# Optimization experiments

Hardware: AMD Instinct MI355X
Metric: run time of the kernel (lower is better)

The kernel has to match this reference:

```python
import jax, jax.numpy as jnp
import numpy as np

EMBED = 1024
HEADS = 16
HEAD_DIM = EMBED // HEADS


def setup_inputs() -> dict:
    key = jax.random.key(0)
    ks = jax.random.split(key, 8)
    B, S = 2, 2048
    inp = {
        "values": jax.random.normal(ks[0], (B, S, EMBED), jnp.float32),
        "keys": jax.random.normal(ks[1], (B, S, EMBED), jnp.float32),
        "queries": jax.random.normal(ks[2], (B, S, EMBED), jnp.float32),
        # per-head projection weights (torch Linear: y = x @ W.T), shared across heads
        "Wv": jax.random.normal(ks[3], (HEAD_DIM, HEAD_DIM), jnp.float32) / np.sqrt(HEAD_DIM),
        "Wk": jax.random.normal(ks[4], (HEAD_DIM, HEAD_DIM), jnp.float32) / np.sqrt(HEAD_DIM),
        "Wq": jax.random.normal(ks[5], (HEAD_DIM, HEAD_DIM), jnp.float32) / np.sqrt(HEAD_DIM),
        "Wo": jax.random.normal(ks[6], (EMBED, EMBED), jnp.float32) / np.sqrt(EMBED),
        "bo": jax.random.normal(ks[7], (EMBED,), jnp.float32) * 0.02,
    }
    return inp


def reference(values, keys, queries, Wv, Wk, Wq, Wo, bo):
    B, S, _ = queries.shape
    # split heads: (B, H, S, D)
    def split(x):
        return x.reshape(B, -1, HEADS, HEAD_DIM).transpose(0, 2, 1, 3)
    v, k, q = split(values), split(keys), split(queries)
    # per-head linear projections (no bias): x @ W.T
    v = jnp.einsum('bhsd,ed->bhse', v, Wv)
    k = jnp.einsum('bhsd,ed->bhse', k, Wk)
    q = jnp.einsum('bhsd,ed->bhse', q, Wq)
    # scaled dot-product attention (naive, full matrix)
    scores = jnp.einsum('bhqd,bhkd->bhqk', q, k) / jnp.sqrt(jnp.float32(HEAD_DIM))
    attn = jax.nn.softmax(scores, axis=-1)
    out = jnp.einsum('bhqk,bhkd->bhqd', attn, v)
    # merge heads and output projection
    out = out.transpose(0, 2, 1, 3).reshape(B, S, EMBED)
    return out @ Wo.T + bo
```

## Files before the change

### kernel.cpp

```cpp
#include <hip/hip_runtime.h>
#include <stdint.h>

#define HEADS 16
#define HD    64
#define SEQ   2048
#define BATCH 2
#define EMB   1024

using short8  = __attribute__((ext_vector_type(8))) short;
using float4v = __attribute__((ext_vector_type(4))) float;

__device__ __forceinline__ unsigned int f2bfr(float f) {
    return (__float_as_uint(f) + 0x8000u) >> 16;
}

__device__ __forceinline__ unsigned int dpp_xor1(unsigned int x) {
    return (unsigned int)__builtin_amdgcn_update_dpp(0, (int)x, 0xB1, 0xF, 0xF, true);
}

__global__ __launch_bounds__(256) void cvt_wo_kernel(const float* __restrict__ Wo,
                                                     unsigned short* __restrict__ Wob) {
    int i = (blockIdx.x * 256 + threadIdx.x) * 4;
    float4 v = *(const float4*)(Wo + i);
    uint2 o;
    o.x = f2bfr(v.x) | (f2bfr(v.y) << 16);
    o.y = f2bfr(v.z) | (f2bfr(v.w) << 16);
    *(uint2*)(Wob + i) = o;
}

__global__ __launch_bounds__(256) void proj_kernel(
    const float* __restrict__ Vx, const float* __restrict__ Kx, const float* __restrict__ Qx,
    const float* __restrict__ Wv, const float* __restrict__ Wk, const float* __restrict__ Wq,
    unsigned short* __restrict__ Qp, unsigned short* __restrict__ Kp,
    unsigned short* __restrict__ Vt) {
    __shared__ __align__(16) unsigned short Ws[64 * 72];
    __shared__ __align__(16) unsigned short xs[64 * 72];
    __shared__ __align__(16) unsigned short vt2[64 * 72];

    const int t = threadIdx.x, w = t >> 6, lane = t & 63, cl = lane & 15, quad = lane >> 4;
    const int z  = blockIdx.z;
    const int bh = blockIdx.y;
    const int b  = bh >> 4, h = bh & 15;
    const int s0 = blockIdx.x * 64;

    const float* x = (z == 0) ? Qx : (z == 1) ? Kx : Vx;
    const float* W = (z == 0) ? Wq : (z == 1) ? Wk : Wv;
    const float scale = (z == 0) ? 0.18033688011112044f : 1.0f;

#pragma unroll
    for (int rep = 0; rep < 4; ++rep) {
        int idx = rep * 1024 + t * 4;
        int e = idx >> 6, d0 = idx & 63;
        float4 w4 = *(const float4*)(W + idx);
        uint2 pk;
        pk.x = f2bfr(w4.x * scale) | (f2bfr(w4.y * scale) << 16);
        pk.y = f2bfr(w4.z * scale) | (f2bfr(w4.w * scale) << 16);
        *(uint2*)(&Ws[e * 72 + d0]) = pk;

        int s = e;
        float4 v4 = *(const float4*)(x + (size_t)(b * SEQ + s0 + s) * EMB + h * 64 + d0);
        uint2 px;
        px.x = f2bfr(v4.x) | (f2bfr(v4.y) << 16);
        px.y = f2bfr(v4.z) | (f2bfr(v4.w) << 16);
        *(uint2*)(&xs[s * 72 + d0]) = px;
    }
    __syncthreads();

    short8 a0 = *(const short8*)(&xs[(w * 16 + cl) * 72 + quad * 8]);
    short8 a1 = *(const short8*)(&xs[(w * 16 + cl) * 72 + 32 + quad * 8]);
    float4v c[4];
#pragma unroll
    for (int nt = 0; nt < 4; ++nt) c[nt] = (float4v){0.f, 0.f, 0.f, 0.f};
#pragma unroll
    for (int nt = 0; nt < 4; ++nt) {
        short8 b0 = *(const short8*)(&Ws[(nt * 16 + cl) * 72 + quad * 8]);
        c[nt] = __builtin_amdgcn_mfma_f32_16x16x32_bf16(a0, b0, c[nt], 0, 0, 0);
        short8 b1 = *(const short8*)(&Ws[(nt * 16 + cl) * 72 + 32 + quad * 8]);
        c[nt] = __builtin_amdgcn_mfma_f32_16x16x32_bf16(a1, b1, c[nt], 0, 0, 0);
    }

    if (z < 2) {
#pragma unroll
        for (int nt = 0; nt < 4; ++nt)
#pragma unroll
            for (int r = 0; r < 4; ++r)
                xs[(w * 16 + quad * 4 + r) * 72 + nt * 16 + cl] =
                    (unsigned short)f2bfr(c[nt][r]);
        unsigned short* outp = (z == 0) ? Qp : Kp;
        int sl = w * 16 + (lane >> 2), c0 = (lane & 3) * 16;
        uint4 o0 = *(const uint4*)(&xs[sl * 72 + c0]);
        uint4 o1 = *(const uint4*)(&xs[sl * 72 + c0 + 8]);
        size_t base = ((size_t)bh * SEQ + s0 + sl) * 64 + c0;
        *(uint4*)(outp + base)     = o0;
        *(uint4*)(outp + base + 8) = o1;
    } else {
#pragma unroll
        for (int nt = 0; nt < 4; ++nt)
#pragma unroll
            for (int r = 0; r < 4; ++r)
                vt2[(nt * 16 + cl) * 72 + w * 16 + quad * 4 + r] =
                    (unsigned short)f2bfr(c[nt][r]);
        __syncthreads();
        int e = t >> 2, sc0 = (t & 3) * 16;
        uint4 o0 = *(const uint4*)(&vt2[e * 72 + sc0]);
        uint4 o1 = *(const uint4*)(&vt2[e * 72 + sc0 + 8]);
        size_t base = ((size_t)bh * 64 + e) * SEQ + s0 + sc0;
        *(uint4*)(Vt + base)     = o0;
        *(uint4*)(Vt + base + 8) = o1;
    }
}

__global__ __launch_bounds__(256) void attn_kernel(
    const unsigned short* __restrict__ Qp, const unsigned short* __restrict__ Kp,
    const unsigned short* __restrict__ Vt, unsigned short* __restrict__ AO) {
    __shared__ __align__(16) unsigned short Ks[2][64 * 72];
    __shared__ __align__(16) unsigned short Vs[2][64 * 72];
    __shared__ __align__(16) unsigned short Ps[4][32 * 72];

    const int t = threadIdx.x;
    const int w = t >> 6, lane = t & 63, cl = lane & 15, quad = lane >> 4;
    const int bh = blockIdx.y;
    const int q0 = blockIdx.x * 128;
    const size_t hbase = (size_t)bh * SEQ * 64;
    const unsigned short* Kbase = Kp + hbase;
    const unsigned short* Vbase = Vt + hbase;

    short8 aq[2][2];
#pragma unroll
    for (int qt = 0; qt < 2; ++qt) {
        size_t rbase = hbase + (size_t)(q0 + w * 32 + qt * 16 + cl) * 64 + quad * 8;
        aq[qt][0] = *(const short8*)(Qp + rbase);
        aq[qt][1] = *(const short8*)(Qp + rbase + 32);
    }

    short8 ones;
#pragma unroll
    for (int i = 0; i < 8; ++i) ones[i] = (short)0x3F80;

    float4v acc[2][5];
#pragma unroll
    for (int qt = 0; qt < 2; ++qt)
#pragma unroll
        for (int nt = 0; nt < 5; ++nt) acc[qt][nt] = (float4v){0.f, 0.f, 0.f, 0.f};

    const int srow = t >> 3;
    const int scol = (t & 7) * 8;

    uint4 kreg[2], vreg[2];
#pragma unroll
    for (int p = 0; p < 2; ++p) {
        int row = srow + p * 32;
        kreg[p] = *(const uint4*)(Kbase + row * 64 + scol);
        vreg[p] = *(const uint4*)(Vbase + (size_t)row * SEQ + scol);
    }

    const int even = ((lane & 1) == 0);
    const unsigned int psel = even ? 0x03020706u : 0x07060302u;
    const int evoff = even ? 0 : 16;
    unsigned int* Pw = (unsigned int*)Ps[w];

    for (int kc = 0; kc < SEQ / 64; ++kc) {
        const int buf = kc & 1;
#pragma unroll
        for (int p = 0; p < 2; ++p) {
            int row = srow + p * 32;
            *(uint4*)(&Ks[buf][row * 72 + scol]) = kreg[p];
            *(uint4*)(&Vs[buf][row * 72 + scol]) = vreg[p];
        }
        __syncthreads();
        if (kc + 1 < SEQ / 64) {
#pragma unroll
            for (int p = 0; p < 2; ++p) {
                int row = srow + p * 32;
                kreg[p] = *(const uint4*)(Kbase + (size_t)(kc + 1) * 4096 + row * 64 + scol);
                vreg[p] = *(const uint4*)(Vbase + (size_t)row * SEQ + (kc + 1) * 64 + scol);
            }
        }

        float4v c[2][4];
#pragma unroll
        for (int qt = 0; qt < 2; ++qt)
#pragma unroll
            for (int nt = 0; nt < 4; ++nt) c[qt][nt] = (float4v){0.f, 0.f, 0.f, 0.f};
#pragma unroll
        for (int nt = 0; nt < 4; ++nt) {
            short8 bk0 = *(const short8*)(&Ks[buf][(nt * 16 + cl) * 72 + quad * 8]);
            short8 bk1 = *(const short8*)(&Ks[buf][(nt * 16 + cl) * 72 + 32 + quad * 8]);
            c[0][nt] = __builtin_amdgcn_mfma_f32_16x16x32_bf16(aq[0][0], bk0, c[0][nt], 0, 0, 0);
            c[0][nt] = __builtin_amdgcn_mfma_f32_16x16x32_bf16(aq[0][1], bk1, c[0][nt], 0, 0, 0);
            c[1][nt] = __builtin_amdgcn_mfma_f32_16x16x32_bf16(aq[1][0], bk0, c[1][nt], 0, 0, 0);
            c[1][nt] = __builtin_amdgcn_mfma_f32_16x16x32_bf16(aq[1][1], bk1, c[1][nt], 0, 0, 0);
        }

#pragma unroll
        for (int qt = 0; qt < 2; ++qt) {
#pragma unroll
            for (int r = 0; r < 4; ++r) {
                unsigned int rr[4], wd[4];
#pragma unroll
                for (int nt = 0; nt < 4; ++nt)
                    rr[nt] = __float_as_uint(__builtin_amdgcn_exp2f(c[qt][nt][r])) + 0x8000u;
#pragma unroll
                for (int nt = 0; nt < 4; ++nt) {
                    unsigned int nb = dpp_xor1(rr[nt]);
                    wd[nt] = __builtin_amdgcn_perm(rr[nt], nb, psel);
                }
                unsigned int wa = even ? wd[0] : wd[2];
                unsigned int wb = even ? wd[1] : wd[3];
                int dwbase = (qt * 16 + quad * 4 + r) * 36 + evoff + (cl >> 1);
                Pw[dwbase]     = wa;
                Pw[dwbase + 8] = wb;
            }
        }

#pragma unroll
        for (int s2i = 0; s2i < 2; ++s2i) {
            short8 ap0 = *(const short8*)(&Ps[w][cl * 72 + s2i * 32 + quad * 8]);
            short8 ap1 = *(const short8*)(&Ps[w][(16 + cl) * 72 + s2i * 32 + quad * 8]);
#pragma unroll
            for (int nt = 0; nt < 4; ++nt) {
                short8 bv = *(const short8*)(&Vs[buf][(nt * 16 + cl) * 72 + s2i * 32 + quad * 8]);
                acc[0][nt] = __builtin_amdgcn_mfma_f32_16x16x32_bf16(ap0, bv, acc[0][nt], 0, 0, 0);
                acc[1][nt] = __builtin_amdgcn_mfma_f32_16x16x32_bf16(ap1, bv, acc[1][nt], 0, 0, 0);
            }
            acc[0][4] = __builtin_amdgcn_mfma_f32_16x16x32_bf16(ap0, ones, acc[0][4], 0, 0, 0);
            acc[1][4] = __builtin_amdgcn_mfma_f32_16x16x32_bf16(ap1, ones, acc[1][4], 0, 0, 0);
        }
    }

#pragma unroll
    for (int qt = 0; qt < 2; ++qt) {
        float inv[4];
#pragma unroll
        for (int r = 0; r < 4; ++r) inv[r] = 1.0f / acc[qt][4][r];
#pragma unroll
        for (int nt = 0; nt < 4; ++nt) {
#pragma unroll
            for (int r = 0; r < 4; ++r) {
                int row = q0 + w * 32 + qt * 16 + quad * 4 + r;
                AO[hbase + (size_t)row * 64 + nt * 16 + cl] =
                    (unsigned short)f2bfr(acc[qt][nt][r] * inv[r]);
            }
        }
    }
}

__global__ __launch_bounds__(256) void outproj_kernel(
    const unsigned short* __restrict__ AO, const unsigned short* __restrict__ Wob,
    const float* __restrict__ bo, float* __restrict__ out) {
    __shared__ __align__(16) unsigned short As[2][64 * 72];
    __shared__ __align__(16) unsigned short Bs[2][64 * 72];

    const int t = threadIdx.x, w = t >> 6, lane = t & 63, cl = lane & 15, quad = lane >> 4;
    const int e0 = blockIdx.x * 64;
    const int m0 = blockIdx.y * 64;
    const int srow = t >> 3, scol = (t & 7) * 8;

    float4v c[4];
#pragma unroll
    for (int nt = 0; nt < 4; ++nt) c[nt] = (float4v){0.f, 0.f, 0.f, 0.f};

    uint4 areg[2], breg[2];
#pragma unroll
    for (int p = 0; p < 2; ++p) {
        int i = srow + p * 32;
        int r = m0 + i, b = r >> 11, s = r & 2047;
        areg[p] = *(const uint4*)(AO + ((size_t)(b * 16 + 0) * SEQ + s) * 64 + scol);
        breg[p] = *(const uint4*)(Wob + (size_t)(e0 + i) * EMB + scol);
    }

    for (int hc = 0; hc < 16; ++hc) {
        const int buf = hc & 1;
#pragma unroll
        for (int p = 0; p < 2; ++p) {
            int i = srow + p * 32;
            *(uint4*)(&As[buf][i * 72 + scol]) = areg[p];
            *(uint4*)(&Bs[buf][i * 72 + scol]) = breg[p];
        }
        __syncthreads();
        if (hc + 1 < 16) {
#pragma unroll
            for (int p = 0; p < 2; ++p) {
                int i = srow + p * 32;
                int r = m0 + i, b = r >> 11, s = r & 2047;
                areg[p] = *(const uint4*)(AO + ((size_t)(b * 16 + hc + 1) * SEQ + s) * 64 + scol);
                breg[p] = *(const uint4*)(Wob + (size_t)(e0 + i) * EMB + (hc + 1) * 64 + scol);
            }
        }
#pragma unroll
        for (int s2i = 0; s2i < 2; ++s2i) {
            short8 a = *(const short8*)(&As[buf][(w * 16 + cl) * 72 + s2i * 32 + quad * 8]);
#pragma unroll
            for (int nt = 0; nt < 4; ++nt) {
                short8 bb = *(const short8*)(&Bs[buf][(nt * 16 + cl) * 72 + s2i * 32 + quad * 8]);
                c[nt] = __builtin_amdgcn_mfma_f32_16x16x32_bf16(a, bb, c[nt], 0, 0, 0);
            }
        }
    }

#pragma unroll
    for (int nt = 0; nt < 4; ++nt) {
        float bias = bo[e0 + nt * 16 + cl];
#pragma unroll
        for (int r = 0; r < 4; ++r) {
            int row = m0 + w * 16 + quad * 4 + r;
            out[(size_t)row * EMB + e0 + nt * 16 + cl] = c[nt][r] + bias;
        }
    }
}

extern "C" void kernel_launch(void* const* d_in, const int* in_sizes, int n_in,
                              void* d_out, int out_size, void* d_ws, size_t ws_size,
                              hipStream_t stream) {
    const float* values  = (const float*)d_in[0];
    const float* keys    = (const float*)d_in[1];
    const float* queries = (const float*)d_in[2];
    const float* Wv = (const float*)d_in[3];
    const float* Wk = (const float*)d_in[4];
    const float* Wq = (const float*)d_in[5];
    const float* Wo = (const float*)d_in[6];
    const float* bo = (const float*)d_in[7];
    float* out = (float*)d_out;

    char* ws = (char*)d_ws;
    unsigned short* Qp  = (unsigned short*)(ws);
    unsigned short* Kp  = (unsigned short*)(ws + (8u  << 20));
    unsigned short* Vt  = (unsigned short*)(ws + (16u << 20));
    unsigned short* AO  = (unsigned short*)(ws + (24u << 20));
    unsigned short* Wob = (unsigned short*)(ws + (32u << 20));

    cvt_wo_kernel<<<dim3(1024), dim3(256), 0, stream>>>(Wo, Wob);
    proj_kernel<<<dim3(SEQ / 64, BATCH * HEADS, 3), dim3(256), 0, stream>>>(
        values, keys, queries, Wv, Wk, Wq, Qp, Kp, Vt);
    attn_kernel<<<dim3(SEQ / 128, BATCH * HEADS), dim3(256), 0, stream>>>(Qp, Kp, Vt, AO);
    outproj_kernel<<<dim3(EMB / 64, (BATCH * SEQ) / 64), dim3(256), 0, stream>>>(
        AO, Wob, bo, out);
}
```

Before: 262.6 us.

## Load K/V fragments directly from global in attention, fuse Wo conversion into projection

The attention kernel no longer stages K and V tiles through shared memory with double buffering and block barriers. Each wave now loads its MFMA B-operand fragments straight from global memory, relying on L1/L2 reuse across the four waves. The P write layout is changed to match, the grid is transposed so blocks sharing a head run together, and launch bounds request two blocks per CU. The separate Wo-to-bf16 conversion kernel is folded into the projection launch as an extra z slice, saving one launch. The risk is redundant global/L2 traffic, since every wave now reloads the same K/V data.

```diff
diff --git a/kernel.cpp b/kernel.cpp
--- a/kernel.cpp
+++ b/kernel.cpp
@@ -18,21 +18,12 @@
     return (unsigned int)__builtin_amdgcn_update_dpp(0, (int)x, 0xB1, 0xF, 0xF, true);
 }
 
-__global__ __launch_bounds__(256) void cvt_wo_kernel(const float* __restrict__ Wo,
-                                                     unsigned short* __restrict__ Wob) {
-    int i = (blockIdx.x * 256 + threadIdx.x) * 4;
-    float4 v = *(const float4*)(Wo + i);
-    uint2 o;
-    o.x = f2bfr(v.x) | (f2bfr(v.y) << 16);
-    o.y = f2bfr(v.z) | (f2bfr(v.w) << 16);
-    *(uint2*)(Wob + i) = o;
-}
-
 __global__ __launch_bounds__(256) void proj_kernel(
     const float* __restrict__ Vx, const float* __restrict__ Kx, const float* __restrict__ Qx,
     const float* __restrict__ Wv, const float* __restrict__ Wk, const float* __restrict__ Wq,
+    const float* __restrict__ Wo,
     unsigned short* __restrict__ Qp, unsigned short* __restrict__ Kp,
-    unsigned short* __restrict__ Vt) {
+    unsigned short* __restrict__ Vt, unsigned short* __restrict__ Wob) {
     __shared__ __align__(16) unsigned short Ws[64 * 72];
     __shared__ __align__(16) unsigned short xs[64 * 72];
     __shared__ __align__(16) unsigned short vt2[64 * 72];
@@ -42,6 +33,16 @@
     const int bh = blockIdx.y;
     const int b  = bh >> 4, h = bh & 15;
     const int s0 = blockIdx.x * 64;
+
+    if (z == 3) {
+        int idx = (bh * 32 + blockIdx.x) * 1024 + t * 4;
+        float4 v = *(const float4*)(Wo + idx);
+        uint2 o;
+        o.x = f2bfr(v.x) | (f2bfr(v.y) << 16);
+        o.y = f2bfr(v.z) | (f2bfr(v.w) << 16);
+        *(uint2*)(Wob + idx) = o;
+        return;
+    }
 
     const float* x = (z == 0) ? Qx : (z == 1) ? Kx : Vx;
     const float* W = (z == 0) ? Wq : (z == 1) ? Wk : Wv;
@@ -110,17 +111,15 @@
     }
 }
 
-__global__ __launch_bounds__(256) void attn_kernel(
+__global__ __launch_bounds__(256, 2) void attn_kernel(
     const unsigned short* __restrict__ Qp, const unsigned short* __restrict__ Kp,
     const unsigned short* __restrict__ Vt, unsigned short* __restrict__ AO) {
-    __shared__ __align__(16) unsigned short Ks[2][64 * 72];
-    __shared__ __align__(16) unsigned short Vs[2][64 * 72];
     __shared__ __align__(16) unsigned short Ps[4][32 * 72];
 
     const int t = threadIdx.x;
     const int w = t >> 6, lane = t & 63, cl = lane & 15, quad = lane >> 4;
-    const int bh = blockIdx.y;
-    const int q0 = blockIdx.x * 128;
+    const int bh = blockIdx.x;
+    const int q0 = blockIdx.y * 128;
     const size_t hbase = (size_t)bh * SEQ * 64;
     const unsigned short* Kbase = Kp + hbase;
     const unsigned short* Vbase = Vt + hbase;
@@ -143,37 +142,23 @@
 #pragma unroll
         for (int nt = 0; nt < 5; ++nt) acc[qt][nt] = (float4v){0.f, 0.f, 0.f, 0.f};
 
-    const int srow = t >> 3;
-    const int scol = (t & 7) * 8;
-
-    uint4 kreg[2], vreg[2];
-#pragma unroll
-    for (int p = 0; p < 2; ++p) {
-        int row = srow + p * 32;
-        kreg[p] = *(const uint4*)(Kbase + row * 64 + scol);
-        vreg[p] = *(const uint4*)(Vbase + (size_t)row * SEQ + scol);
-    }
-
     const int even = ((lane & 1) == 0);
     const unsigned int psel = even ? 0x03020706u : 0x07060302u;
-    const int evoff = even ? 0 : 16;
+    const int evoff = even ? 0 : 8;
     unsigned int* Pw = (unsigned int*)Ps[w];
 
+    const unsigned short* kptr = Kbase + (size_t)(cl * 64 + quad * 8);
+    const unsigned short* vptr = Vbase + (size_t)cl * SEQ + quad * 8;
+
+#pragma unroll 2
     for (int kc = 0; kc < SEQ / 64; ++kc) {
-        const int buf = kc & 1;
-#pragma unroll
-        for (int p = 0; p < 2; ++p) {
-            int row = srow + p * 32;
-            *(uint4*)(&Ks[buf][row * 72 + scol]) = kreg[p];
-            *(uint4*)(&Vs[buf][row * 72 + scol]) = vreg[p];
-        }
-        __syncthreads();
-        if (kc + 1 < SEQ / 64) {
-#pragma unroll
-            for (int p = 0; p < 2; ++p) {
-                int row = srow + p * 32;
-                kreg[p] = *(const uint4*)(Kbase + (size_t)(kc + 1) * 4096 + row * 64 + scol);
-                vreg[p] = *(const uint4*)(Vbase + (size_t)row * SEQ + (kc + 1) * 64 + scol);
+        short8 kf[4][2], vf[4][2];
+#pragma unroll
+        for (int nt = 0; nt < 4; ++nt) {
+#pragma unroll
+            for (int s2 = 0; s2 < 2; ++s2) {
+                kf[nt][s2] = *(const short8*)(kptr + (size_t)(kc * 64 + nt * 16) * 64 + s2 * 32);
+                vf[nt][s2] = *(const short8*)(vptr + (size_t)(nt * 16) * SEQ + kc * 64 + s2 * 32);
             }
         }
 
@@ -184,12 +169,10 @@
             for (int nt = 0; nt < 4; ++nt) c[qt][nt] = (float4v){0.f, 0.f, 0.f, 0.f};
 #pragma unroll
         for (int nt = 0; nt < 4; ++nt) {
-            short8 bk0 = *(const short8*)(&Ks[buf][(nt * 16 + cl) * 72 + quad * 8]);
-            short8 bk1 = *(const short8*)(&Ks[buf][(nt * 16 + cl) * 72 + 32 + quad * 8]);
-            c[0][nt] = __builtin_amdgcn_mfma_f32_16x16x32_bf16(aq[0][0], bk0, c[0][nt], 0, 0, 0);
-            c[0][nt] = __builtin_amdgcn_mfma_f32_16x16x32_bf16(aq[0][1], bk1, c[0][nt], 0, 0, 0);
-            c[1][nt] = __builtin_amdgcn_mfma_f32_16x16x32_bf16(aq[1][0], bk0, c[1][nt], 0, 0, 0);
-            c[1][nt] = __builtin_amdgcn_mfma_f32_16x16x32_bf16(aq[1][1], bk1, c[1][nt], 0, 0, 0);
+            c[0][nt] = __builtin_amdgcn_mfma_f32_16x16x32_bf16(aq[0][0], kf[nt][0], c[0][nt], 0, 0, 0);
+            c[0][nt] = __builtin_amdgcn_mfma_f32_16x16x32_bf16(aq[0][1], kf[nt][1], c[0][nt], 0, 0, 0);
+            c[1][nt] = __builtin_amdgcn_mfma_f32_16x16x32_bf16(aq[1][0], kf[nt][0], c[1][nt], 0, 0, 0);
+            c[1][nt] = __builtin_amdgcn_mfma_f32_16x16x32_bf16(aq[1][1], kf[nt][1], c[1][nt], 0, 0, 0);
         }
 
 #pragma unroll
@@ -205,11 +188,11 @@
                     unsigned int nb = dpp_xor1(rr[nt]);
                     wd[nt] = __builtin_amdgcn_perm(rr[nt], nb, psel);
                 }
-                unsigned int wa = even ? wd[0] : wd[2];
-                unsigned int wb = even ? wd[1] : wd[3];
+                unsigned int wa = even ? wd[0] : wd[1];
+                unsigned int wb = even ? wd[2] : wd[3];
                 int dwbase = (qt * 16 + quad * 4 + r) * 36 + evoff + (cl >> 1);
-                Pw[dwbase]     = wa;
-                Pw[dwbase + 8] = wb;
+                Pw[dwbase]      = wa;
+                Pw[dwbase + 16] = wb;
             }
         }
 
@@ -219,9 +202,8 @@
             short8 ap1 = *(const short8*)(&Ps[w][(16 + cl) * 72 + s2i * 32 + quad * 8]);
 #pragma unroll
             for (int nt = 0; nt < 4; ++nt) {
-                short8 bv = *(const short8*)(&Vs[buf][(nt * 16 + cl) * 72 + s2i * 32 + quad * 8]);
-                acc[0][nt] = __builtin_amdgcn_mfma_f32_16x16x32_bf16(ap0, bv, acc[0][nt], 0, 0, 0);
-                acc[1][nt] = __builtin_amdgcn_mfma_f32_16x16x32_bf16(ap1, bv, acc[1][nt], 0, 0, 0);
+                acc[0][nt] = __builtin_amdgcn_mfma_f32_16x16x32_bf16(ap0, vf[nt][s2i], acc[0][nt], 0, 0, 0);
+                acc[1][nt] = __builtin_amdgcn_mfma_f32_16x16x32_bf16(ap1, vf[nt][s2i], acc[1][nt], 0, 0, 0);
             }
             acc[0][4] = __builtin_amdgcn_mfma_f32_16x16x32_bf16(ap0, ones, acc[0][4], 0, 0, 0);
             acc[1][4] = __builtin_amdgcn_mfma_f32_16x16x32_bf16(ap1, ones, acc[1][4], 0, 0, 0);
@@ -329,10 +311,9 @@
     unsigned short* AO  = (unsigned short*)(ws + (24u << 20));
     unsigned short* Wob = (unsigned short*)(ws + (32u << 20));
 
-    cvt_wo_kernel<<<dim3(1024), dim3(256), 0, stream>>>(Wo, Wob);
-    proj_kernel<<<dim3(SEQ / 64, BATCH * HEADS, 3), dim3(256), 0, stream>>>(
-        values, keys, queries, Wv, Wk, Wq, Qp, Kp, Vt);
-    attn_kernel<<<dim3(SEQ / 128, BATCH * HEADS), dim3(256), 0, stream>>>(Qp, Kp, Vt, AO);
+    proj_kernel<<<dim3(SEQ / 64, BATCH * HEADS, 4), dim3(256), 0, stream>>>(
+        values, keys, queries, Wv, Wk, Wq, Wo, Qp, Kp, Vt, Wob);
+    attn_kernel<<<dim3(BATCH * HEADS, SEQ / 128), dim3(256), 0, stream>>>(Qp, Kp, Vt, AO);
     outproj_kernel<<<dim3(EMB / 64, (BATCH * SEQ) / 64), dim3(256), 0, stream>>>(
         AO, Wob, bo, out);
 }
```

Result: slower. 307.8 us (+17.2%).
